# Optimization experiments

Measured on AMD Instinct MI355X. Metric: run time of the kernel, lower is better.

Reference implementation:

```python
import jax, jax.numpy as jnp
import numpy as np

STRIDE = 2
CAPS_DIM = 8  # out_channels: capsule dimensionality
EPS = 1e-8


def _squash(s):
    # Canonical capsule squash along the last (capsule-dim) axis:
    # v = (||s||^2 / (1 + ||s||^2)) * s / ||s||
    sq_norm = jnp.sum(s * s, axis=-1, keepdims=True)  # [B, N, 1]
    scale = sq_norm / (1.0 + sq_norm) / jnp.sqrt(sq_norm + EPS)
    return scale * s


def setup_inputs() -> dict:
    key = jax.random.key(0)
    kx, kw = jax.random.split(key)
    x = jax.random.normal(kx, (64, 256, 40, 40), dtype=jnp.float32)
    W = jax.random.normal(kw, (256, 256, 9, 9), dtype=jnp.float32) * 0.02
    b = jnp.zeros((256,), dtype=jnp.float32)
    return {"x": x, "W": W, "b": b}


def reference(x, W, b):
    # Conv2d: NCHW input, OIHW kernel, stride 2, VALID padding -> (64,256,16,16)
    out = jax.lax.conv_general_dilated(
        x, W,
        window_strides=(STRIDE, STRIDE),
        padding="VALID",
        dimension_numbers=("NCHW", "OIHW", "NCHW"),
    ) + b[None, :, None, None]
    batch_size = out.shape[0]
    caps = out.reshape(batch_size, -1, CAPS_DIM)  # (64, 8192, 8)
    return _squash(caps)
```

## Files before the change

kernel.cpp:

```cpp
#include <hip/hip_runtime.h>


typedef __attribute__((ext_vector_type(8))) short bf16x8;
typedef __attribute__((ext_vector_type(4))) float f32x4;

#define SBAR __builtin_amdgcn_sched_barrier(0)
#define HBAR __builtin_amdgcn_s_barrier()
#define CFEN asm volatile("" ::: "memory")

static __device__ __forceinline__ unsigned short f2bf(float f) {
  unsigned u = __builtin_bit_cast(unsigned, f);
  u += 0x7FFFu + ((u >> 16) & 1u);
  return (unsigned short)(u >> 16);
}

static __device__ __forceinline__ void gll16(const void* g, void* l) {
  typedef __attribute__((address_space(1))) const unsigned char AS1;
  typedef __attribute__((address_space(3))) unsigned char AS3;
  __builtin_amdgcn_global_load_lds((AS1*)g, (AS3*)l, 16, 0, 0);
}

__global__ __launch_bounds__(256) void prep_k(const float* __restrict__ x,
                                              const float* __restrict__ W,
                                              unsigned short* __restrict__ Xt,
                                              unsigned short* __restrict__ Wb) {
  __shared__ float t[5184];
  int bx = blockIdx.x;
  if (bx < 10240) {
    int ict = bx & 3;
    int ih = (bx >> 2) % 40;
    int b  = bx / 160;
    const float4* src4 = (const float4*)(x + ((size_t)(b * 256 + ict * 64) * 40 + ih) * 40);
    for (int i = threadIdx.x; i < 640; i += 256) {
      int ic = i / 10, q = i - ic * 10;
      float4 v = src4[ic * 400 + q];
      float* tr = t + ic * 41 + q * 4;
      tr[0] = v.x; tr[1] = v.y; tr[2] = v.z; tr[3] = v.w;
    }
    __syncthreads();
    unsigned short* dst = Xt + ((size_t)(b * 40 + ih) * 40) * 256 + ict * 64;
    for (int i = threadIdx.x; i < 1280; i += 256) {
      int iw = i >> 5, icp = i & 31;
      unsigned lo = f2bf(t[(icp * 2) * 41 + iw]);
      unsigned hi = f2bf(t[(icp * 2 + 1) * 41 + iw]);
      *(unsigned*)(dst + (size_t)iw * 256 + icp * 2) = (hi << 16) | lo;
    }
  } else {
    int bid = bx - 10240;
    int oc = bid >> 2, ict = bid & 3;
    const float* src = W + ((size_t)oc * 256 + (size_t)ict * 64) * 81;
    for (int i = threadIdx.x; i < 5184; i += 256) t[i] = src[i];
    __syncthreads();
    unsigned short* dst = Wb + (size_t)oc * 20736 + ict * 64;
    for (int i = threadIdx.x; i < 5184; i += 256) {
      int khw = i >> 6, ic = i & 63;
      dst[(size_t)khw * 256 + ic] = f2bf(t[ic * 81 + khw]);
    }
  }
}

__global__ __launch_bounds__(512, 2) void gemm_k(const unsigned short* __restrict__ Wb,
                                                 const unsigned short* __restrict__ Xt,
                                                 float* __restrict__ Cp, int kts) {
  __shared__ __align__(16) short LDS[65536];
  const int tid = threadIdx.x;
  const int l = tid & 63, w = tid >> 6;
  const int wm = w >> 2, wn = w & 3;
  const int nc = blockIdx.x, sz = blockIdx.z;

  const int lrow = l >> 3, lslot = l & 7;
  const int chunk = (lslot ^ lrow) << 3;

  unsigned aoffA[2], boffB[2];
  int dstA[2], dstB[2];
#pragma unroll
  for (int h = 0; h < 2; ++h) {
    int srow = h * 128 + w * 16 + lrow;
    aoffA[h] = (unsigned)srow * 20736u + (unsigned)chunk;
    int oh = h * 8 + w, ow = lrow;
    boffB[h] = (unsigned)((nc * 40 + 2 * oh) * 40 + 2 * ow) * 256u + (unsigned)chunk;
    dstA[h] = (h * 128 + w * 16) << 6;
    dstB[h] = 32768 + dstA[h];
  }

  const int fr = l & 15, kq = l >> 4, sw = fr & 7;
  const int arow0 = wm * 128 + fr;
  const int brow0 = wn * 64 + fr;

  f32x4 acc[8][4];
#pragma unroll
  for (int mi = 0; mi < 8; ++mi)
#pragma unroll
    for (int ni = 0; ni < 4; ++ni) acc[mi][ni] = (f32x4){0.f, 0.f, 0.f, 0.f};

  const int kt0 = sz * kts, nkt = kts;

  {
    const unsigned ka0 = (unsigned)kt0 << 6;
    const int khw0 = kt0 >> 2, ict0 = kt0 & 3;
    const int kh0 = khw0 / 9, kw0 = khw0 - kh0 * 9;
    const unsigned kb0 = (unsigned)((kh0 * 40 + kw0) << 8) + (unsigned)(ict0 << 6);
#pragma unroll
    for (int h = 0; h < 2; ++h) {
      gll16(Wb + aoffA[h] + ka0, LDS + dstA[h]);
      gll16(Wb + aoffA[h] + ka0 + 8u * 20736u, LDS + dstA[h] + 512);
      gll16(Xt + boffB[h] + kb0, LDS + dstB[h]);
      gll16(Xt + boffB[h] + kb0 + 4096u, LDS + dstB[h] + 512);
    }
  }

#define DO_PHASE(P)                                                              \
  {                                                                              \
    bf16x8 af[2][2];                                                             \
    _Pragma("unroll") for (int j = 0; j < 2; ++j)                                \
    _Pragma("unroll") for (int kk = 0; kk < 2; ++kk) {                           \
      int row = arow0 + (2 * (P) + j) * 16;                                      \
      int kc = kk * 4 + kq;                                                      \
      af[j][kk] = *(const bf16x8*)(LDS + buf + (row << 6) + ((kc ^ sw) << 3));   \
    }                                                                            \
    __builtin_amdgcn_s_setprio(1);                                               \
    _Pragma("unroll") for (int j = 0; j < 2; ++j)                                \
    _Pragma("unroll") for (int ni = 0; ni < 4; ++ni)                             \
    _Pragma("unroll") for (int kk = 0; kk < 2; ++kk)                             \
      acc[2 * (P) + j][ni] = __builtin_amdgcn_mfma_f32_16x16x32_bf16(            \
          af[j][kk], bg[ni][kk], acc[2 * (P) + j][ni], 0, 0, 0);                 \
    __builtin_amdgcn_s_setprio(0);                                               \
  }

  for (int t = 0; t < nkt; ++t) {
    const int kt = kt0 + t;
    const int buf = (t & 1) << 14;
    const int nb = buf ^ 16384;
    const unsigned kaN = (unsigned)(kt + 1) << 6;
    const int ktn = kt + 1;
    const int khwN = ktn >> 2, ictN = ktn & 3;
    const int khN = khwN / 9, kwN = khwN - khN * 9;
    const unsigned kbN = (unsigned)((khN * 40 + kwN) << 8) + (unsigned)(ictN << 6);
    const bool more = (t + 1 < nkt);

    SBAR; HBAR; CFEN;
    if (more) {
#pragma unroll
      for (int h = 0; h < 2; ++h) {
        gll16(Wb + aoffA[h] + kaN, LDS + nb + dstA[h]);
        gll16(Wb + aoffA[h] + kaN + 8u * 20736u, LDS + nb + dstA[h] + 512);
        gll16(Xt + boffB[h] + kbN, LDS + nb + dstB[h]);
        gll16(Xt + boffB[h] + kbN + 4096u, LDS + nb + dstB[h] + 512);
      }
      SBAR;
      asm volatile("s_waitcnt vmcnt(8)" ::: "memory");
    } else {
      SBAR;
      asm volatile("s_waitcnt vmcnt(0)" ::: "memory");
    }
    HBAR; CFEN; SBAR;

    bf16x8 bg[4][2];
#pragma unroll
    for (int ni = 0; ni < 4; ++ni)
#pragma unroll
      for (int kk = 0; kk < 2; ++kk) {
        int row = brow0 + ni * 16;
        int kc = kk * 4 + kq;
        bg[ni][kk] = *(const bf16x8*)(LDS + 32768 + buf + (row << 6) + ((kc ^ sw) << 3));
      }

    DO_PHASE(0)
    DO_PHASE(1)
    DO_PHASE(2)
    DO_PHASE(3)
  }
#undef DO_PHASE

  float* Co = Cp + (size_t)sz * 4194304;
#pragma unroll
  for (int mi = 0; mi < 8; ++mi) {
#pragma unroll
    for (int ni = 0; ni < 4; ++ni) {
      int oc = wm * 128 + mi * 16 + kq * 4;
      int n = (nc << 8) + wn * 64 + ni * 16 + fr;
#pragma unroll
      for (int r = 0; r < 4; ++r)
        Co[(size_t)(oc + r) * 16384 + n] = acc[mi][ni][r];
    }
  }
}

__global__ __launch_bounds__(256) void finish_k(const float* __restrict__ Cp,
                                                const float* __restrict__ bias,
                                                float* __restrict__ out, int S) {
  int cap = blockIdx.x * 256 + threadIdx.x;
  int b = cap >> 13;
  int flat = (cap & 8191) << 3;
  int oc = flat >> 8;
  size_t cbase = (size_t)oc * 16384 + (size_t)b * 256 + (size_t)(flat & 255);
  float v[8];
#pragma unroll
  for (int i = 0; i < 8; ++i) v[i] = 0.f;
  for (int s = 0; s < S; ++s) {
    const float4* p = (const float4*)(Cp + (size_t)s * 4194304 + cbase);
    float4 a0 = p[0], a1 = p[1];
    v[0] += a0.x; v[1] += a0.y; v[2] += a0.z; v[3] += a0.w;
    v[4] += a1.x; v[5] += a1.y; v[6] += a1.z; v[7] += a1.w;
  }
  float bb = bias[oc];
  float sq = 0.f;
#pragma unroll
  for (int i = 0; i < 8; ++i) { v[i] += bb; sq += v[i] * v[i]; }
  float scale = sq / ((1.0f + sq) * sqrtf(sq + 1e-8f));
  float4 o0 = make_float4(v[0] * scale, v[1] * scale, v[2] * scale, v[3] * scale);
  float4 o1 = make_float4(v[4] * scale, v[5] * scale, v[6] * scale, v[7] * scale);
  float4* q = (float4*)(out + (size_t)cap * 8);
  q[0] = o0; q[1] = o1;
}

extern "C" void kernel_launch(void* const* d_in, const int* in_sizes, int n_in,
                              void* d_out, int out_size, void* d_ws, size_t ws_size,
                              hipStream_t stream) {
  const float* x    = (const float*)d_in[0];
  const float* W    = (const float*)d_in[1];
  const float* bias = (const float*)d_in[2];
  float* out = (float*)d_out;
  char* ws = (char*)d_ws;

  unsigned short* Xt = (unsigned short*)ws;
  unsigned short* Wb = (unsigned short*)(ws + 52428800ull);
  float*          Cp = (float*)(ws + 63045632ull);

  const size_t slice = 16777216ull;
  int S = 1;
  if (ws_size >= 63045632ull + 4 * slice) S = 4;
  else if (ws_size >= 63045632ull + 2 * slice) S = 2;

  prep_k<<<11264, 256, 0, stream>>>(x, W, Xt, Wb);
  gemm_k<<<dim3(64, 1, S), 512, 0, stream>>>(Wb, Xt, Cp, 324 / S);
  finish_k<<<2048, 256, 0, stream>>>(Cp, bias, out, S);
}
```

Baseline: 341.1 us.

## Drop split-K partials, fuse bias+squash into GEMM epilogue, vectorize input transpose

Replaces the split-K GEMM with 256x256 tiles and its separate reduction/squash kernel by a single-pass GEMM. It uses 128x128 tiles, 256 blocks of 4 waves, runs the full K loop in each block, and grid-swizzles the block index. Bias and squash are applied in the epilogue, with the 8-element capsule norm reduced by lane shuffles. This removes the write and re-read of the fp32 partial-sum slices and one kernel launch. The input transpose kernel now handles all 256 channels per block and stores packed 16-byte bf16 vectors. The trade-off is lower per-CU wave occupancy and more LDS traffic per FLOP from the smaller tiles.

```diff
diff --git a/kernel.cpp b/kernel.cpp
--- a/kernel.cpp
+++ b/kernel.cpp
@@ -24,29 +24,35 @@
                                               const float* __restrict__ W,
                                               unsigned short* __restrict__ Xt,
                                               unsigned short* __restrict__ Wb) {
-  __shared__ float t[5184];
+  __shared__ float t[10496];
   int bx = blockIdx.x;
-  if (bx < 10240) {
-    int ict = bx & 3;
-    int ih = (bx >> 2) % 40;
-    int b  = bx / 160;
-    const float4* src4 = (const float4*)(x + ((size_t)(b * 256 + ict * 64) * 40 + ih) * 40);
-    for (int i = threadIdx.x; i < 640; i += 256) {
-      int ic = i / 10, q = i - ic * 10;
+  if (bx < 2560) {
+    int b = bx / 40, ih = bx - b * 40;
+    const float4* src4 = (const float4*)(x + (size_t)b * 409600 + (size_t)ih * 40);
+#pragma unroll
+    for (int j = 0; j < 10; ++j) {
+      int idx = j * 256 + threadIdx.x;
+      int ic = idx / 10, q = idx - ic * 10;
       float4 v = src4[ic * 400 + q];
       float* tr = t + ic * 41 + q * 4;
       tr[0] = v.x; tr[1] = v.y; tr[2] = v.z; tr[3] = v.w;
     }
     __syncthreads();
-    unsigned short* dst = Xt + ((size_t)(b * 40 + ih) * 40) * 256 + ict * 64;
-    for (int i = threadIdx.x; i < 1280; i += 256) {
-      int iw = i >> 5, icp = i & 31;
-      unsigned lo = f2bf(t[(icp * 2) * 41 + iw]);
-      unsigned hi = f2bf(t[(icp * 2 + 1) * 41 + iw]);
-      *(unsigned*)(dst + (size_t)iw * 256 + icp * 2) = (hi << 16) | lo;
+    unsigned short* dst = Xt + ((size_t)(b * 40 + ih) * 40) * 256;
+#pragma unroll
+    for (int j = 0; j < 5; ++j) {
+      int idx = j * 256 + threadIdx.x;
+      int iw = idx >> 5, g = idx & 31;
+      const float* col = t + g * 8 * 41 + iw;
+      unsigned p0 = f2bf(col[0])      | ((unsigned)f2bf(col[41])  << 16);
+      unsigned p1 = f2bf(col[82])     | ((unsigned)f2bf(col[123]) << 16);
+      unsigned p2 = f2bf(col[164])    | ((unsigned)f2bf(col[205]) << 16);
+      unsigned p3 = f2bf(col[246])    | ((unsigned)f2bf(col[287]) << 16);
+      uint4 pk = make_uint4(p0, p1, p2, p3);
+      *(uint4*)(dst + (size_t)iw * 256 + g * 8) = pk;
     }
   } else {
-    int bid = bx - 10240;
+    int bid = bx - 2560;
     int oc = bid >> 2, ict = bid & 3;
     const float* src = W + ((size_t)oc * 256 + (size_t)ict * 64) * 81;
     for (int i = threadIdx.x; i < 5184; i += 256) t[i] = src[i];
@@ -59,93 +65,63 @@
   }
 }
 
-__global__ __launch_bounds__(512, 2) void gemm_k(const unsigned short* __restrict__ Wb,
+__global__ __launch_bounds__(256, 2) void gemm_k(const unsigned short* __restrict__ Wb,
                                                  const unsigned short* __restrict__ Xt,
-                                                 float* __restrict__ Cp, int kts) {
-  __shared__ __align__(16) short LDS[65536];
+                                                 const float* __restrict__ bias,
+                                                 float* __restrict__ out) {
+  __shared__ __align__(16) short LDS[32768];
   const int tid = threadIdx.x;
   const int l = tid & 63, w = tid >> 6;
-  const int wm = w >> 2, wn = w & 3;
-  const int nc = blockIdx.x, sz = blockIdx.z;
+  const int wm = w >> 1, wn = w & 1;
+  const int idx = ((blockIdx.x & 7) << 5) + (blockIdx.x >> 3);
+  const int bm = idx & 1, bn = idx >> 1;
 
   const int lrow = l >> 3, lslot = l & 7;
   const int chunk = (lslot ^ lrow) << 3;
 
-  unsigned aoffA[2], boffB[2];
-  int dstA[2], dstB[2];
-#pragma unroll
-  for (int h = 0; h < 2; ++h) {
-    int srow = h * 128 + w * 16 + lrow;
-    aoffA[h] = (unsigned)srow * 20736u + (unsigned)chunk;
-    int oh = h * 8 + w, ow = lrow;
-    boffB[h] = (unsigned)((nc * 40 + 2 * oh) * 40 + 2 * ow) * 256u + (unsigned)chunk;
-    dstA[h] = (h * 128 + w * 16) << 6;
-    dstB[h] = 32768 + dstA[h];
+  unsigned aoff[4], boff[4];
+  int dstT[4];
+#pragma unroll
+  for (int h = 0; h < 4; ++h) {
+    int r = w * 32 + h * 8 + lrow;
+    aoff[h] = (unsigned)(bm * 128 + r) * 20736u + (unsigned)chunk;
+    int b = bn >> 1;
+    int oh = ((bn & 1) << 3) + (r >> 4), ow = r & 15;
+    boff[h] = (unsigned)((b * 40 + 2 * oh) * 40 + 2 * ow) * 256u + (unsigned)chunk;
+    dstT[h] = (w * 32 + h * 8) << 6;
   }
 
   const int fr = l & 15, kq = l >> 4, sw = fr & 7;
-  const int arow0 = wm * 128 + fr;
+  const int arow0 = wm * 64 + fr;
   const int brow0 = wn * 64 + fr;
 
-  f32x4 acc[8][4];
-#pragma unroll
-  for (int mi = 0; mi < 8; ++mi)
+  f32x4 acc[4][4];
+#pragma unroll
+  for (int mi = 0; mi < 4; ++mi)
 #pragma unroll
     for (int ni = 0; ni < 4; ++ni) acc[mi][ni] = (f32x4){0.f, 0.f, 0.f, 0.f};
 
-  const int kt0 = sz * kts, nkt = kts;
-
-  {
-    const unsigned ka0 = (unsigned)kt0 << 6;
-    const int khw0 = kt0 >> 2, ict0 = kt0 & 3;
-    const int kh0 = khw0 / 9, kw0 = khw0 - kh0 * 9;
-    const unsigned kb0 = (unsigned)((kh0 * 40 + kw0) << 8) + (unsigned)(ict0 << 6);
-#pragma unroll
-    for (int h = 0; h < 2; ++h) {
-      gll16(Wb + aoffA[h] + ka0, LDS + dstA[h]);
-      gll16(Wb + aoffA[h] + ka0 + 8u * 20736u, LDS + dstA[h] + 512);
-      gll16(Xt + boffB[h] + kb0, LDS + dstB[h]);
-      gll16(Xt + boffB[h] + kb0 + 4096u, LDS + dstB[h] + 512);
-    }
-  }
-
-#define DO_PHASE(P)                                                              \
-  {                                                                              \
-    bf16x8 af[2][2];                                                             \
-    _Pragma("unroll") for (int j = 0; j < 2; ++j)                                \
-    _Pragma("unroll") for (int kk = 0; kk < 2; ++kk) {                           \
-      int row = arow0 + (2 * (P) + j) * 16;                                      \
-      int kc = kk * 4 + kq;                                                      \
-      af[j][kk] = *(const bf16x8*)(LDS + buf + (row << 6) + ((kc ^ sw) << 3));   \
-    }                                                                            \
-    __builtin_amdgcn_s_setprio(1);                                               \
-    _Pragma("unroll") for (int j = 0; j < 2; ++j)                                \
-    _Pragma("unroll") for (int ni = 0; ni < 4; ++ni)                             \
-    _Pragma("unroll") for (int kk = 0; kk < 2; ++kk)                             \
-      acc[2 * (P) + j][ni] = __builtin_amdgcn_mfma_f32_16x16x32_bf16(            \
-          af[j][kk], bg[ni][kk], acc[2 * (P) + j][ni], 0, 0, 0);                 \
-    __builtin_amdgcn_s_setprio(0);                                               \
-  }
-
-  for (int t = 0; t < nkt; ++t) {
-    const int kt = kt0 + t;
-    const int buf = (t & 1) << 14;
-    const int nb = buf ^ 16384;
-    const unsigned kaN = (unsigned)(kt + 1) << 6;
-    const int ktn = kt + 1;
+#pragma unroll
+  for (int h = 0; h < 4; ++h) {
+    gll16(Wb + aoff[h], LDS + dstT[h]);
+    gll16(Xt + boff[h], LDS + 16384 + dstT[h]);
+  }
+
+  for (int t = 0; t < 324; ++t) {
+    const int buf = (t & 1) << 13;
+    const int nb = buf ^ 8192;
+    const int ktn = t + 1;
+    const unsigned kaN = (unsigned)ktn << 6;
     const int khwN = ktn >> 2, ictN = ktn & 3;
     const int khN = khwN / 9, kwN = khwN - khN * 9;
     const unsigned kbN = (unsigned)((khN * 40 + kwN) << 8) + (unsigned)(ictN << 6);
-    const bool more = (t + 1 < nkt);
 
     SBAR; HBAR; CFEN;
-    if (more) {
-#pragma unroll
-      for (int h = 0; h < 2; ++h) {
-        gll16(Wb + aoffA[h] + kaN, LDS + nb + dstA[h]);
-        gll16(Wb + aoffA[h] + kaN + 8u * 20736u, LDS + nb + dstA[h] + 512);
-        gll16(Xt + boffB[h] + kbN, LDS + nb + dstB[h]);
-        gll16(Xt + boffB[h] + kbN + 4096u, LDS + nb + dstB[h] + 512);
+    if (t < 323) {
+#pragma unroll
+      for (int h = 0; h < 4; ++h) {
+        gll16(Wb + aoff[h] + kaN, LDS + nb + dstT[h]);
+        gll16(Xt + boff[h] + kbN, LDS + 16384 + nb + dstT[h]);
       }
       SBAR;
       asm volatile("s_waitcnt vmcnt(8)" ::: "memory");
@@ -162,56 +138,51 @@
       for (int kk = 0; kk < 2; ++kk) {
         int row = brow0 + ni * 16;
         int kc = kk * 4 + kq;
-        bg[ni][kk] = *(const bf16x8*)(LDS + 32768 + buf + (row << 6) + ((kc ^ sw) << 3));
-      }
-
-    DO_PHASE(0)
-    DO_PHASE(1)
-    DO_PHASE(2)
-    DO_PHASE(3)
-  }
-#undef DO_PHASE
-
-  float* Co = Cp + (size_t)sz * 4194304;
-#pragma unroll
-  for (int mi = 0; mi < 8; ++mi) {
+        bg[ni][kk] = *(const bf16x8*)(LDS + 16384 + buf + (row << 6) + ((kc ^ sw) << 3));
+      }
+#pragma unroll
+    for (int mi = 0; mi < 4; ++mi) {
+      bf16x8 af[2];
+#pragma unroll
+      for (int kk = 0; kk < 2; ++kk) {
+        int row = arow0 + mi * 16;
+        int kc = kk * 4 + kq;
+        af[kk] = *(const bf16x8*)(LDS + buf + (row << 6) + ((kc ^ sw) << 3));
+      }
+      __builtin_amdgcn_s_setprio(1);
+#pragma unroll
+      for (int ni = 0; ni < 4; ++ni)
+#pragma unroll
+        for (int kk = 0; kk < 2; ++kk)
+          acc[mi][ni] = __builtin_amdgcn_mfma_f32_16x16x32_bf16(af[kk], bg[ni][kk],
+                                                                acc[mi][ni], 0, 0, 0);
+      __builtin_amdgcn_s_setprio(0);
+    }
+  }
+
+  const int n0 = bn << 7;
+#pragma unroll
+  for (int mi = 0; mi < 4; ++mi) {
+    int oc = bm * 128 + wm * 64 + mi * 16 + kq * 4;
+    float bb[4];
+#pragma unroll
+    for (int r = 0; r < 4; ++r) bb[r] = bias[oc + r];
 #pragma unroll
     for (int ni = 0; ni < 4; ++ni) {
-      int oc = wm * 128 + mi * 16 + kq * 4;
-      int n = (nc << 8) + wn * 64 + ni * 16 + fr;
-#pragma unroll
-      for (int r = 0; r < 4; ++r)
-        Co[(size_t)(oc + r) * 16384 + n] = acc[mi][ni][r];
-    }
-  }
-}
-
-__global__ __launch_bounds__(256) void finish_k(const float* __restrict__ Cp,
-                                                const float* __restrict__ bias,
-                                                float* __restrict__ out, int S) {
-  int cap = blockIdx.x * 256 + threadIdx.x;
-  int b = cap >> 13;
-  int flat = (cap & 8191) << 3;
-  int oc = flat >> 8;
-  size_t cbase = (size_t)oc * 16384 + (size_t)b * 256 + (size_t)(flat & 255);
-  float v[8];
-#pragma unroll
-  for (int i = 0; i < 8; ++i) v[i] = 0.f;
-  for (int s = 0; s < S; ++s) {
-    const float4* p = (const float4*)(Cp + (size_t)s * 4194304 + cbase);
-    float4 a0 = p[0], a1 = p[1];
-    v[0] += a0.x; v[1] += a0.y; v[2] += a0.z; v[3] += a0.w;
-    v[4] += a1.x; v[5] += a1.y; v[6] += a1.z; v[7] += a1.w;
-  }
-  float bb = bias[oc];
-  float sq = 0.f;
-#pragma unroll
-  for (int i = 0; i < 8; ++i) { v[i] += bb; sq += v[i] * v[i]; }
-  float scale = sq / ((1.0f + sq) * sqrtf(sq + 1e-8f));
-  float4 o0 = make_float4(v[0] * scale, v[1] * scale, v[2] * scale, v[3] * scale);
-  float4 o1 = make_float4(v[4] * scale, v[5] * scale, v[6] * scale, v[7] * scale);
-  float4* q = (float4*)(out + (size_t)cap * 8);
-  q[0] = o0; q[1] = o1;
+      int n = n0 + wn * 64 + ni * 16 + fr;
+      float* o = out + ((size_t)(n >> 8) << 16) + (size_t)oc * 256 + (n & 255);
+#pragma unroll
+      for (int r = 0; r < 4; ++r) {
+        float v = acc[mi][ni][r] + bb[r];
+        float s2 = v * v;
+        s2 += __shfl_xor(s2, 1, 64);
+        s2 += __shfl_xor(s2, 2, 64);
+        s2 += __shfl_xor(s2, 4, 64);
+        float sc = s2 / ((1.0f + s2) * sqrtf(s2 + 1e-8f));
+        o[r * 256] = v * sc;
+      }
+    }
+  }
 }
 
 extern "C" void kernel_launch(void* const* d_in, const int* in_sizes, int n_in,
@@ -225,14 +196,7 @@
 
   unsigned short* Xt = (unsigned short*)ws;
   unsigned short* Wb = (unsigned short*)(ws + 52428800ull);
-  float*          Cp = (float*)(ws + 63045632ull);
-
-  const size_t slice = 16777216ull;
-  int S = 1;
-  if (ws_size >= 63045632ull + 4 * slice) S = 4;
-  else if (ws_size >= 63045632ull + 2 * slice) S = 2;
-
-  prep_k<<<11264, 256, 0, stream>>>(x, W, Xt, Wb);
-  gemm_k<<<dim3(64, 1, S), 512, 0, stream>>>(Wb, Xt, Cp, 324 / S);
-  finish_k<<<2048, 256, 0, stream>>>(Cp, bias, out, S);
-}
+
+  prep_k<<<3584, 256, 0, stream>>>(x, W, Xt, Wb);
+  gemm_k<<<256, 256, 0, stream>>>(Wb, Xt, bias, out);
+}
```

After: 388.5 us. 13.9% more time.
